# Kernel optimization log

Measured on AMD Instinct MI355X. Metric: run time of the kernel, lower is better.

## Reference

```python
import jax, jax.numpy as jnp
import numpy as np

K = 8
LN_EPS = 1e-5


def setup_inputs() -> dict:
    key = jax.random.key(0)
    ks = jax.random.split(key, 12)
    Nq, N, d = 2048, 50000, 256
    xav = np.sqrt(6.0 / (d + d)).astype(np.float32)
    inp = {
        "query": jax.random.normal(ks[0], (Nq, d), jnp.float32),
        "query_pos": jax.random.uniform(ks[1], (Nq, 3), jnp.float32) * 10.0,
        "inst_feats": jax.random.normal(ks[2], (N, d), jnp.float32),
        "sp_coords": jax.random.uniform(ks[3], (N, 3), jnp.float32) * 10.0,
        "w_q": jax.random.uniform(ks[4], (d, d), jnp.float32, -xav, xav),
        "w_v": jax.random.uniform(ks[5], (d, d), jnp.float32, -xav, xav),
        "w_o": jax.random.uniform(ks[6], (d, d), jnp.float32, -xav, xav),
        # original inits w_k/w_b to zero (uniform gate); use small random for a nontrivial gate
        "w_k": jax.random.normal(ks[7], (K, d), jnp.float32) * 0.02,
        "w_b": jax.random.normal(ks[8], (K,), jnp.float32) * 0.02,
        "gamma": jnp.ones((d,), jnp.float32),
        "beta": jnp.zeros((d,), jnp.float32),
    }
    return inp


def _knn_idx(query_pos, sp_coords, k):
    # squared euclidean distances [Nq, N] via ||q||^2 - 2 q.p + ||p||^2
    d2 = (
        jnp.sum(query_pos * query_pos, -1, keepdims=True)
        - 2.0 * (query_pos @ sp_coords.T)
        + jnp.sum(sp_coords * sp_coords, -1)[None, :]
    )
    _, idx = jax.lax.top_k(-d2, k)  # [Nq, k] nearest-neighbor indices
    return idx


def reference(query, query_pos, inst_feats, sp_coords, w_q, w_v, w_o, w_k, w_b, gamma, beta):
    idx = _knn_idx(query_pos, sp_coords, K)
    feat = inst_feats[idx]                       # [Nq, k, d] gathered neighbor feats
    q = query @ w_q.T                            # [Nq, d]
    v = feat @ w_v.T                             # [Nq, k, d]
    gate = jax.nn.softmax(q @ w_k.T + w_b, -1)   # [Nq, k]
    w = jnp.einsum("qk,qkd->qd", gate, q[:, None, :] * v)
    out = w @ w_o.T + query                      # dropout p=0 -> identity; residual
    mu = jnp.mean(out, -1, keepdims=True)
    var = jnp.mean((out - mu) ** 2, -1, keepdims=True)
    return (out - mu) * jax.lax.rsqrt(var + LN_EPS) * gamma + beta
```

## Files before the change

kernel.cpp:

```cpp
#include <hip/hip_runtime.h>
#include <math.h>

#define D        256
#define KNN      8
#define G        16
#define NCELL    (G*G*G)
#define CS       0.625f
#define EPS_D2   2e-3f
#define CAP      64
#define SPILLMAX 50000

typedef unsigned long long u64;
typedef __attribute__((ext_vector_type(8))) short bf16x8;
typedef __attribute__((ext_vector_type(4))) float f32x4;

__device__ __forceinline__ unsigned short f2b(float f) {
    unsigned u = __float_as_uint(f);
    u += 0x7fff + ((u >> 16) & 1);
    return (unsigned short)(u >> 16);
}
__device__ __forceinline__ bf16x8 pack8(float4 a, float4 b) {
    bf16x8 r;
    r[0] = (short)f2b(a.x); r[1] = (short)f2b(a.y);
    r[2] = (short)f2b(a.z); r[3] = (short)f2b(a.w);
    r[4] = (short)f2b(b.x); r[5] = (short)f2b(b.y);
    r[6] = (short)f2b(b.z); r[7] = (short)f2b(b.w);
    return r;
}

__device__ __forceinline__ unsigned enc_f32(float f) {
    unsigned b = __float_as_uint(f);
    return b ^ ((unsigned)(((int)b) >> 31) | 0x80000000u);
}
__device__ __forceinline__ float dec_f32(unsigned t) {
    unsigned m = (unsigned)(((int)t) >> 31);
    return __uint_as_float(t ^ (0x80000000u | ~m));
}
__device__ __forceinline__ u64 mkkey(float d2, int j) {
    return ((u64)enc_f32(d2) << 32) | (u64)(unsigned)j;
}
__device__ __forceinline__ int cell_of(float x) {
    int c = (int)(x * 1.6f);
    return c < 0 ? 0 : (c > G-1 ? G-1 : c);
}

#define INSERT8(xk)                                                            \
    if ((xk) < k7) {                                                           \
        const bool c0 = (xk) < k0, c1 = (xk) < k1, c2 = (xk) < k2,             \
                   c3 = (xk) < k3, c4 = (xk) < k4, c5 = (xk) < k5,             \
                   c6 = (xk) < k6;                                             \
        k7 = c6 ? k6 : (xk);                                                   \
        k6 = c5 ? k5 : (c6 ? (xk) : k6);                                       \
        k5 = c4 ? k4 : (c5 ? (xk) : k5);                                       \
        k4 = c3 ? k3 : (c4 ? (xk) : k4);                                       \
        k3 = c2 ? k2 : (c3 ? (xk) : k3);                                       \
        k2 = c1 ? k1 : (c2 ? (xk) : k2);                                       \
        k1 = c0 ? k0 : (c1 ? (xk) : k1);                                       \
        k0 = c0 ? (xk) : k0;                                                   \
    }

#define SCORE(p)                                                               \
    {                                                                          \
        const float sp  = __fadd_rn(__fadd_rn(__fmul_rn((p).x,(p).x),          \
                                  __fmul_rn((p).y,(p).y)), __fmul_rn((p).z,(p).z)); \
        const float dot = __fmaf_rn(qz,(p).z, __fmaf_rn(qy,(p).y, __fmul_rn(qx,(p).x))); \
        const float d2  = __fadd_rn(__fsub_rn(sq, __fmul_rn(2.0f, dot)), sp);  \
        const u64 xk = mkkey(d2, __float_as_int((p).w));                       \
        INSERT8(xk)                                                            \
    }

__device__ __forceinline__ void wave_merge8(int l, u64& k0, u64& k1, u64& k2, u64& k3,
                                            u64& k4, u64& k5, u64& k6, u64& k7,
                                            u64& mine)
{
#pragma unroll
    for (int rd = 0; rd < KNN; ++rd) {
        u64 m = k0;
#pragma unroll
        for (int o = 32; o; o >>= 1) {
            const u64 t = __shfl_xor(m, o);
            if (t < m) m = t;
        }
        if (k0 == m) {
            k0 = k1; k1 = k2; k2 = k3; k3 = k4; k4 = k5; k5 = k6; k6 = k7;
            k7 = ~0ull;
        }
        if (l == rd) mine = m;
    }
}

__global__ __launch_bounds__(256) void prep(const float* __restrict__ w_k,
                                            const float* __restrict__ w_q,
                                            const float* __restrict__ w_v,
                                            const float* __restrict__ w_o,
                                            float* __restrict__ wk2,
                                            unsigned short* __restrict__ wqs,
                                            unsigned short* __restrict__ wvs,
                                            unsigned short* __restrict__ wos,
                                            int4* __restrict__ cnt4,
                                            int* __restrict__ spill_cnt)
{
    const int b = blockIdx.x, t = threadIdx.x;
    if (b < 8) {
        float acc = 0.f;
#pragma unroll 8
        for (int d = 0; d < D; ++d)
            acc = fmaf(w_k[b*D + d], w_q[(size_t)d*D + t], acc);
        wk2[b*D + t] = acc;
    } else if (b < 12) {
        cnt4[(b-8)*256 + t] = make_int4(0, 0, 0, 0);
        if (b == 8 && t == 0) *spill_cnt = 0;
    } else {
        const int m = (b - 12) >> 5;
        const int local = (b - 12) & 31;
        const int idx = local * 256 + t;
        const int nt = idx >> 9;
        const int ks = (idx >> 6) & 7;
        const int l  = idx & 63;
        const int col = nt*16 + (l & 15);
        const int k   = ks*32 + (l >> 4)*8;
        const float* src = (m == 0) ? w_q : (m == 1) ? w_v : w_o;
        unsigned short* dst = (m == 0) ? wqs : (m == 1) ? wvs : wos;
        const float4 x0 = *(const float4*)&src[(size_t)col*D + k];
        const float4 x1 = *(const float4*)&src[(size_t)col*D + k + 4];
        *(bf16x8*)&dst[(size_t)idx * 8] = pack8(x0, x1);
    }
}

__global__ __launch_bounds__(256) void scatter_bins(const float* __restrict__ spc,
                                                    int* __restrict__ cnt,
                                                    float4* __restrict__ bins,
                                                    int* __restrict__ spill_cnt,
                                                    float4* __restrict__ spill, int N)
{
    const int j = blockIdx.x * 256 + threadIdx.x;
    if (j >= N) return;
    const float px = spc[3*j+0], py = spc[3*j+1], pz = spc[3*j+2];
    const int cell = cell_of(px) | (cell_of(py) << 4) | (cell_of(pz) << 8);
    const float4 p = make_float4(px, py, pz, __int_as_float(j));
    const int pos = atomicAdd(&cnt[cell], 1);
    if (pos < CAP) bins[cell*CAP + pos] = p;
    else {
        const int sp = atomicAdd(spill_cnt, 1);
        if (sp < SPILLMAX) spill[sp] = p;
    }
}

__device__ __forceinline__ void knn_gate_wave(int q, int l,
                                              const float* __restrict__ qpos,
                                              const float4* __restrict__ bins,
                                              const int* __restrict__ cnt,
                                              const int* __restrict__ spill_cnt,
                                              const float4* __restrict__ spill,
                                              const float* __restrict__ query,
                                              const float* __restrict__ wk2,
                                              const float* __restrict__ w_b,
                                              const float* __restrict__ feats,
                                              float4& qv_out, float4& fb_out)
{
    const float qx = qpos[3*q+0], qy = qpos[3*q+1], qz = qpos[3*q+2];
    const float sq = __fadd_rn(__fadd_rn(__fmul_rn(qx,qx), __fmul_rn(qy,qy)),
                               __fmul_rn(qz,qz));
    const int cx = cell_of(qx), cy = cell_of(qy), cz = cell_of(qz);

    auto bstart = [](int c, float coord) {
        const float f = coord * 1.6f - (float)c;
        int b = c + ((f < 0.5f) ? -2 : -1);
        return b < 0 ? 0 : (b > G-4 ? G-4 : b);
    };
    const int bx = bstart(cx, qx), by = bstart(cy, qy), bz = bstart(cz, qz);

    u64 k0 = ~0ull, k1 = ~0ull, k2 = ~0ull, k3 = ~0ull,
        k4 = ~0ull, k5 = ~0ull, k6 = ~0ull, k7 = ~0ull;

    {
        const int x = bx + (l & 3), y = by + ((l >> 2) & 3), z = bz + (l >> 4);
        const int ci = x | (y << 4) | (z << 8);
        const int n = min(cnt[ci], CAP);
        const int st = ci * CAP;
        for (int i = 0; i < n; ++i) { const float4 p = bins[st + i]; SCORE(p) }
    }
    {
        const int ns = min(*spill_cnt, SPILLMAX);
        for (int i = l; i < ns; i += 64) { const float4 p = spill[i]; SCORE(p) }
    }

    u64 mine = ~0ull;
    wave_merge8(l, k0, k1, k2, k3, k4, k5, k6, k7, mine);
    const u64 worst = __shfl(mine, KNN-1);

    const float w8 = dec_f32((unsigned)(worst >> 32));
    float dmin = INFINITY;
    if (bx > 0)     dmin = fminf(dmin, qx - (float)bx * CS);
    if (bx + 4 < G) dmin = fminf(dmin, (float)(bx + 4) * CS - qx);
    if (by > 0)     dmin = fminf(dmin, qy - (float)by * CS);
    if (by + 4 < G) dmin = fminf(dmin, (float)(by + 4) * CS - qy);
    if (bz > 0)     dmin = fminf(dmin, qz - (float)bz * CS);
    if (bz + 4 < G) dmin = fminf(dmin, (float)(bz + 4) * CS - qz);

    if (!(w8 + EPS_D2 <= dmin * dmin)) {
        k0 = (l < KNN) ? mine : ~0ull;
        k1 = ~0ull; k2 = ~0ull; k3 = ~0ull; k4 = ~0ull;
        k5 = ~0ull; k6 = ~0ull; k7 = ~0ull;
        for (int c = l; c < NCELL; c += 64) {
            const int x = c & 15, y = (c >> 4) & 15, z = c >> 8;
            if (x >= bx && x < bx+4 && y >= by && y < by+4 && z >= bz && z < bz+4) continue;
            const int n = min(cnt[c], CAP);
            const int st = c * CAP;
            for (int i = 0; i < n; ++i) { const float4 p = bins[st + i]; SCORE(p) }
        }
        wave_merge8(l, k0, k1, k2, k3, k4, k5, k6, k7, mine);
    }

    int ids[KNN];
    const int my_id = (int)(unsigned)(mine & 0xffffffffu);
#pragma unroll
    for (int j = 0; j < KNN; ++j) ids[j] = __shfl(my_id, j);

    const float4 qv = *(const float4*)&query[(size_t)q*D + l*4];
    float logit[KNN];
#pragma unroll
    for (int j = 0; j < KNN; ++j) {
        const float4 w = *(const float4*)&wk2[(size_t)j*D + l*4];
        logit[j] = fmaf(qv.x, w.x, fmaf(qv.y, w.y, fmaf(qv.z, w.z, qv.w*w.w)));
    }
#pragma unroll
    for (int o = 32; o; o >>= 1) {
#pragma unroll
        for (int j = 0; j < KNN; ++j) logit[j] += __shfl_xor(logit[j], o);
    }
#pragma unroll
    for (int j = 0; j < KNN; ++j) logit[j] += w_b[j];

    float m = logit[0];
#pragma unroll
    for (int j = 1; j < KNN; ++j) m = fmaxf(m, logit[j]);
    float e[KNN]; float ssum = 0.f;
#pragma unroll
    for (int j = 0; j < KNN; ++j) { e[j] = expf(logit[j] - m); ssum += e[j]; }
    const float inv = 1.f / ssum;

    float4 acc4 = make_float4(0.f, 0.f, 0.f, 0.f);
#pragma unroll
    for (int j = 0; j < KNN; ++j) {
        const float gj = e[j] * inv;
        const float4 f = *(const float4*)&feats[(size_t)ids[j]*D + l*4];
        acc4.x = fmaf(gj, f.x, acc4.x);
        acc4.y = fmaf(gj, f.y, acc4.y);
        acc4.z = fmaf(gj, f.z, acc4.z);
        acc4.w = fmaf(gj, f.w, acc4.w);
    }
    qv_out = qv;
    fb_out = acc4;
}

__global__ __launch_bounds__(512) void mega6(const float* __restrict__ qpos,
                                             const float4* __restrict__ bins,
                                             const int* __restrict__ cnt,
                                             const int* __restrict__ spill_cnt,
                                             const float4* __restrict__ spill,
                                             const float* __restrict__ query,
                                             const float* __restrict__ wk2,
                                             const float* __restrict__ w_b,
                                             const float* __restrict__ feats,
                                             const unsigned short* __restrict__ wqs,
                                             const unsigned short* __restrict__ wvs,
                                             const unsigned short* __restrict__ wos,
                                             const float* __restrict__ gmm,
                                             const float* __restrict__ bta,
                                             float* __restrict__ out)
{
    __shared__ unsigned short a_lds[16][264];
    __shared__ unsigned short f_lds[16][264];
    __shared__ unsigned short w_lds[16][264];
    __shared__ float q_f32[8][260];
    __shared__ float o_f32[8][260];

    const int tid = threadIdx.x;
    const int wv  = tid >> 6, l = tid & 63;
    const int r0  = blockIdx.x * 8;

    {
        const int arr = tid >> 8;
        const int row = 8 + ((tid >> 5) & 7);
        const int o8  = (tid & 31) * 8;
        const bf16x8 z = {0,0,0,0,0,0,0,0};
        if (arr == 0) *(bf16x8*)&a_lds[row][o8] = z;
        else          *(bf16x8*)&f_lds[row][o8] = z;
    }

    {
        float4 qv, fb;
        knn_gate_wave(r0 + wv, l, qpos, bins, cnt, spill_cnt, spill,
                      query, wk2, w_b, feats, qv, fb);
        *(float4*)&q_f32[wv][l*4] = qv;
        short4 qb; qb.x = (short)f2b(qv.x); qb.y = (short)f2b(qv.y);
                   qb.z = (short)f2b(qv.z); qb.w = (short)f2b(qv.w);
        *(short4*)&a_lds[wv][l*4] = qb;
        short4 fv; fv.x = (short)f2b(fb.x); fv.y = (short)f2b(fb.y);
                   fv.z = (short)f2b(fb.z); fv.w = (short)f2b(fb.w);
        *(short4*)&f_lds[wv][l*4] = fv;
    }
    __syncthreads();

    const int mrow = l & 15;
    const int kq   = (l >> 4) * 8;

    f32x4 aq[2], av[2];
#pragma unroll
    for (int t = 0; t < 2; ++t) {
        aq[t] = (f32x4){0.f, 0.f, 0.f, 0.f};
        av[t] = (f32x4){0.f, 0.f, 0.f, 0.f};
    }
#pragma unroll
    for (int ks = 0; ks < 8; ++ks) {
        const bf16x8 af = *(const bf16x8*)&a_lds[mrow][ks*32 + kq];
        const bf16x8 ff = *(const bf16x8*)&f_lds[mrow][ks*32 + kq];
#pragma unroll
        for (int t = 0; t < 2; ++t) {
            const int nt = wv*2 + t;
            const size_t fo = ((size_t)(nt*8 + ks)*64 + l) * 8;
            const bf16x8 bq = *(const bf16x8*)&wqs[fo];
            const bf16x8 bv = *(const bf16x8*)&wvs[fo];
            aq[t] = __builtin_amdgcn_mfma_f32_16x16x32_bf16(af, bq, aq[t], 0, 0, 0);
            av[t] = __builtin_amdgcn_mfma_f32_16x16x32_bf16(ff, bv, av[t], 0, 0, 0);
        }
    }
#pragma unroll
    for (int t = 0; t < 2; ++t) {
#pragma unroll
        for (int r = 0; r < 4; ++r) {
            const int row = (l >> 4) * 4 + r;
            const int col = wv*32 + t*16 + (l & 15);
            w_lds[row][col] = f2b(aq[t][r] * av[t][r]);
        }
    }
    __syncthreads();

    f32x4 ao[2];
#pragma unroll
    for (int t = 0; t < 2; ++t) ao[t] = (f32x4){0.f, 0.f, 0.f, 0.f};
#pragma unroll
    for (int ks = 0; ks < 8; ++ks) {
        const bf16x8 wf = *(const bf16x8*)&w_lds[mrow][ks*32 + kq];
#pragma unroll
        for (int t = 0; t < 2; ++t) {
            const int nt = wv*2 + t;
            const size_t fo = ((size_t)(nt*8 + ks)*64 + l) * 8;
            const bf16x8 bo = *(const bf16x8*)&wos[fo];
            ao[t] = __builtin_amdgcn_mfma_f32_16x16x32_bf16(wf, bo, ao[t], 0, 0, 0);
        }
    }
#pragma unroll
    for (int t = 0; t < 2; ++t) {
#pragma unroll
        for (int r = 0; r < 4; ++r) {
            const int row = (l >> 4) * 4 + r;
            if (row < 8) {
                const int col = wv*32 + t*16 + (l & 15);
                o_f32[row][col] = ao[t][r] + q_f32[row][col];
            }
        }
    }
    __syncthreads();

    {
        const float4 v = *(const float4*)&o_f32[wv][l*4];
        float s  = (v.x + v.y) + (v.z + v.w);
        float s2 = fmaf(v.x, v.x, fmaf(v.y, v.y, fmaf(v.z, v.z, v.w*v.w)));
#pragma unroll
        for (int o = 32; o; o >>= 1) { s += __shfl_xor(s, o); s2 += __shfl_xor(s2, o); }
        const float mu  = s * (1.f/256.f);
        const float var = fmaf(s2, 1.f/256.f, -mu*mu);
        const float rs  = rsqrtf(var + 1e-5f);
        const float4 g = *(const float4*)&gmm[l*4];
        const float4 b = *(const float4*)&bta[l*4];
        float4 o4;
        o4.x = (v.x - mu) * rs * g.x + b.x;
        o4.y = (v.y - mu) * rs * g.y + b.y;
        o4.z = (v.z - mu) * rs * g.z + b.z;
        o4.w = (v.w - mu) * rs * g.w + b.w;
        *(float4*)&out[(size_t)(r0+wv)*D + l*4] = o4;
    }
}

extern "C" void kernel_launch(void* const* d_in, const int* in_sizes, int n_in,
                              void* d_out, int out_size, void* d_ws, size_t ws_size,
                              hipStream_t stream)
{
    const float* query = (const float*)d_in[0];
    const float* qpos  = (const float*)d_in[1];
    const float* feats = (const float*)d_in[2];
    const float* spc   = (const float*)d_in[3];
    const float* w_q   = (const float*)d_in[4];
    const float* w_v   = (const float*)d_in[5];
    const float* w_o   = (const float*)d_in[6];
    const float* w_k   = (const float*)d_in[7];
    const float* w_b   = (const float*)d_in[8];
    const float* gamma = (const float*)d_in[9];
    const float* beta  = (const float*)d_in[10];

    const int Nq = in_sizes[0] / D;
    const int N  = in_sizes[2] / D;

    char* ws = (char*)d_ws;
    size_t off = 0;
    int* cnt = (int*)(ws + off);               off += ((size_t)NCELL * 4 + 255) & ~(size_t)255;
    int* spill_cnt = (int*)(ws + off);         off += 256;
    float* wk2 = (float*)(ws + off);           off += ((size_t)KNN * D * 4 + 255) & ~(size_t)255;
    unsigned short* wqs = (unsigned short*)(ws + off); off += (size_t)D * D * 2;
    unsigned short* wvs = (unsigned short*)(ws + off); off += (size_t)D * D * 2;
    unsigned short* wos = (unsigned short*)(ws + off); off += (size_t)D * D * 2;
    float4* bins = (float4*)(ws + off);        off += ((size_t)NCELL * CAP * 16 + 255) & ~(size_t)255;
    float4* spill = (float4*)(ws + off);       off += ((size_t)SPILLMAX * 16 + 255) & ~(size_t)255;

    prep<<<108, 256, 0, stream>>>(w_k, w_q, w_v, w_o, wk2, wqs, wvs, wos,
                                  (int4*)cnt, spill_cnt);
    scatter_bins<<<(N + 255)/256, 256, 0, stream>>>(spc, cnt, bins, spill_cnt, spill, N);
    mega6<<<Nq/8, 512, 0, stream>>>(qpos, bins, cnt, spill_cnt, spill,
                                    query, wk2, w_b, feats, wqs, wvs, wos,
                                    gamma, beta, (float*)d_out);
}
```

Baseline: 45.48 us.

## Split each query's KNN cell scan across two waves and merge via LDS

The fused kernel now handles 4 queries per block instead of 8, with two waves per query. Each wave scans half of the 64 candidate cells, and two lanes share each cell by taking alternating points. The two partial top-8 lists are merged through shared memory by one wave, which then handles the fallback full scan, the gate and the feature gather. This shortens the serial per-lane scan loop and doubles the grid size. In exchange it adds a block barrier and a merge step, and leaves half the waves idle in the gate and LayerNorm phases, with more padding waste in the MFMA tiles.

Measured after the change: 46.87 us. +3.0%, slower.

```diff
diff --git a/kernel.cpp b/kernel.cpp
--- a/kernel.cpp
+++ b/kernel.cpp
@@ -146,115 +146,7 @@
     }
 }
 
-__device__ __forceinline__ void knn_gate_wave(int q, int l,
-                                              const float* __restrict__ qpos,
-                                              const float4* __restrict__ bins,
-                                              const int* __restrict__ cnt,
-                                              const int* __restrict__ spill_cnt,
-                                              const float4* __restrict__ spill,
-                                              const float* __restrict__ query,
-                                              const float* __restrict__ wk2,
-                                              const float* __restrict__ w_b,
-                                              const float* __restrict__ feats,
-                                              float4& qv_out, float4& fb_out)
-{
-    const float qx = qpos[3*q+0], qy = qpos[3*q+1], qz = qpos[3*q+2];
-    const float sq = __fadd_rn(__fadd_rn(__fmul_rn(qx,qx), __fmul_rn(qy,qy)),
-                               __fmul_rn(qz,qz));
-    const int cx = cell_of(qx), cy = cell_of(qy), cz = cell_of(qz);
-
-    auto bstart = [](int c, float coord) {
-        const float f = coord * 1.6f - (float)c;
-        int b = c + ((f < 0.5f) ? -2 : -1);
-        return b < 0 ? 0 : (b > G-4 ? G-4 : b);
-    };
-    const int bx = bstart(cx, qx), by = bstart(cy, qy), bz = bstart(cz, qz);
-
-    u64 k0 = ~0ull, k1 = ~0ull, k2 = ~0ull, k3 = ~0ull,
-        k4 = ~0ull, k5 = ~0ull, k6 = ~0ull, k7 = ~0ull;
-
-    {
-        const int x = bx + (l & 3), y = by + ((l >> 2) & 3), z = bz + (l >> 4);
-        const int ci = x | (y << 4) | (z << 8);
-        const int n = min(cnt[ci], CAP);
-        const int st = ci * CAP;
-        for (int i = 0; i < n; ++i) { const float4 p = bins[st + i]; SCORE(p) }
-    }
-    {
-        const int ns = min(*spill_cnt, SPILLMAX);
-        for (int i = l; i < ns; i += 64) { const float4 p = spill[i]; SCORE(p) }
-    }
-
-    u64 mine = ~0ull;
-    wave_merge8(l, k0, k1, k2, k3, k4, k5, k6, k7, mine);
-    const u64 worst = __shfl(mine, KNN-1);
-
-    const float w8 = dec_f32((unsigned)(worst >> 32));
-    float dmin = INFINITY;
-    if (bx > 0)     dmin = fminf(dmin, qx - (float)bx * CS);
-    if (bx + 4 < G) dmin = fminf(dmin, (float)(bx + 4) * CS - qx);
-    if (by > 0)     dmin = fminf(dmin, qy - (float)by * CS);
-    if (by + 4 < G) dmin = fminf(dmin, (float)(by + 4) * CS - qy);
-    if (bz > 0)     dmin = fminf(dmin, qz - (float)bz * CS);
-    if (bz + 4 < G) dmin = fminf(dmin, (float)(bz + 4) * CS - qz);
-
-    if (!(w8 + EPS_D2 <= dmin * dmin)) {
-        k0 = (l < KNN) ? mine : ~0ull;
-        k1 = ~0ull; k2 = ~0ull; k3 = ~0ull; k4 = ~0ull;
-        k5 = ~0ull; k6 = ~0ull; k7 = ~0ull;
-        for (int c = l; c < NCELL; c += 64) {
-            const int x = c & 15, y = (c >> 4) & 15, z = c >> 8;
-            if (x >= bx && x < bx+4 && y >= by && y < by+4 && z >= bz && z < bz+4) continue;
-            const int n = min(cnt[c], CAP);
-            const int st = c * CAP;
-            for (int i = 0; i < n; ++i) { const float4 p = bins[st + i]; SCORE(p) }
-        }
-        wave_merge8(l, k0, k1, k2, k3, k4, k5, k6, k7, mine);
-    }
-
-    int ids[KNN];
-    const int my_id = (int)(unsigned)(mine & 0xffffffffu);
-#pragma unroll
-    for (int j = 0; j < KNN; ++j) ids[j] = __shfl(my_id, j);
-
-    const float4 qv = *(const float4*)&query[(size_t)q*D + l*4];
-    float logit[KNN];
-#pragma unroll
-    for (int j = 0; j < KNN; ++j) {
-        const float4 w = *(const float4*)&wk2[(size_t)j*D + l*4];
-        logit[j] = fmaf(qv.x, w.x, fmaf(qv.y, w.y, fmaf(qv.z, w.z, qv.w*w.w)));
-    }
-#pragma unroll
-    for (int o = 32; o; o >>= 1) {
-#pragma unroll
-        for (int j = 0; j < KNN; ++j) logit[j] += __shfl_xor(logit[j], o);
-    }
-#pragma unroll
-    for (int j = 0; j < KNN; ++j) logit[j] += w_b[j];
-
-    float m = logit[0];
-#pragma unroll
-    for (int j = 1; j < KNN; ++j) m = fmaxf(m, logit[j]);
-    float e[KNN]; float ssum = 0.f;
-#pragma unroll
-    for (int j = 0; j < KNN; ++j) { e[j] = expf(logit[j] - m); ssum += e[j]; }
-    const float inv = 1.f / ssum;
-
-    float4 acc4 = make_float4(0.f, 0.f, 0.f, 0.f);
-#pragma unroll
-    for (int j = 0; j < KNN; ++j) {
-        const float gj = e[j] * inv;
-        const float4 f = *(const float4*)&feats[(size_t)ids[j]*D + l*4];
-        acc4.x = fmaf(gj, f.x, acc4.x);
-        acc4.y = fmaf(gj, f.y, acc4.y);
-        acc4.z = fmaf(gj, f.z, acc4.z);
-        acc4.w = fmaf(gj, f.w, acc4.w);
-    }
-    qv_out = qv;
-    fb_out = acc4;
-}
-
-__global__ __launch_bounds__(512) void mega6(const float* __restrict__ qpos,
+__global__ __launch_bounds__(512) void mega7(const float* __restrict__ qpos,
                                              const float4* __restrict__ bins,
                                              const int* __restrict__ cnt,
                                              const int* __restrict__ spill_cnt,
@@ -273,33 +165,149 @@
     __shared__ unsigned short a_lds[16][264];
     __shared__ unsigned short f_lds[16][264];
     __shared__ unsigned short w_lds[16][264];
-    __shared__ float q_f32[8][260];
-    __shared__ float o_f32[8][260];
+    __shared__ float q_f32[4][260];
+    __shared__ float o_f32[4][260];
+    __shared__ u64  cand[4][16];
 
     const int tid = threadIdx.x;
     const int wv  = tid >> 6, l = tid & 63;
-    const int r0  = blockIdx.x * 8;
+    const int qi  = wv >> 1, part = wv & 1;
+    const int r0  = blockIdx.x * 4;
+    const int q   = r0 + qi;
 
     {
-        const int arr = tid >> 8;
-        const int row = 8 + ((tid >> 5) & 7);
-        const int o8  = (tid & 31) * 8;
+        const int o = tid;
+        const int oo = (o < 384) ? o : o - 384;
+        const int row = 4 + (oo >> 5);
+        const int c8 = (oo & 31) * 8;
         const bf16x8 z = {0,0,0,0,0,0,0,0};
-        if (arr == 0) *(bf16x8*)&a_lds[row][o8] = z;
-        else          *(bf16x8*)&f_lds[row][o8] = z;
-    }
+        if (o < 384) *(bf16x8*)&a_lds[row][c8] = z;
+        else         *(bf16x8*)&f_lds[row][c8] = z;
+        if (tid < 256) {
+            const int oo2 = tid + 128;
+            const int row2 = 4 + (oo2 >> 5);
+            const int c82 = (oo2 & 31) * 8;
+            *(bf16x8*)&f_lds[row2][c82] = z;
+        }
+    }
+
+    const float qx = qpos[3*q+0], qy = qpos[3*q+1], qz = qpos[3*q+2];
+    const float sq = __fadd_rn(__fadd_rn(__fmul_rn(qx,qx), __fmul_rn(qy,qy)),
+                               __fmul_rn(qz,qz));
+    const int cx = cell_of(qx), cy = cell_of(qy), cz = cell_of(qz);
+
+    auto bstart = [](int c, float coord) {
+        const float f = coord * 1.6f - (float)c;
+        int b = c + ((f < 0.5f) ? -2 : -1);
+        return b < 0 ? 0 : (b > G-4 ? G-4 : b);
+    };
+    const int bx = bstart(cx, qx), by = bstart(cy, qy), bz = bstart(cz, qz);
+
+    u64 k0 = ~0ull, k1 = ~0ull, k2 = ~0ull, k3 = ~0ull,
+        k4 = ~0ull, k5 = ~0ull, k6 = ~0ull, k7 = ~0ull;
 
     {
-        float4 qv, fb;
-        knn_gate_wave(r0 + wv, l, qpos, bins, cnt, spill_cnt, spill,
-                      query, wk2, w_b, feats, qv, fb);
-        *(float4*)&q_f32[wv][l*4] = qv;
+        const int c = part*32 + (l >> 1), sub = l & 1;
+        const int x = bx + (c & 3), y = by + ((c >> 2) & 3), z = bz + (c >> 4);
+        const int ci = x | (y << 4) | (z << 8);
+        const int n = min(cnt[ci], CAP);
+        const int st = ci * CAP;
+        for (int i = sub; i < n; i += 2) { const float4 p = bins[st + i]; SCORE(p) }
+    }
+    if (part == 0) {
+        const int ns = min(*spill_cnt, SPILLMAX);
+        for (int i = l; i < ns; i += 64) { const float4 p = spill[i]; SCORE(p) }
+    }
+
+    u64 mine = ~0ull;
+    wave_merge8(l, k0, k1, k2, k3, k4, k5, k6, k7, mine);
+    if (l < KNN) cand[qi][part*KNN + l] = mine;
+    __syncthreads();
+
+    if (part == 0) {
+        u64 k = (l < 16) ? cand[qi][l] : ~0ull;
+        u64 m2 = ~0ull;
+#pragma unroll
+        for (int rd = 0; rd < KNN; ++rd) {
+            u64 m = k;
+#pragma unroll
+            for (int o = 32; o; o >>= 1) {
+                const u64 t = __shfl_xor(m, o);
+                if (t < m) m = t;
+            }
+            if (k == m) k = ~0ull;
+            if (l == rd) m2 = m;
+        }
+        const u64 worst = __shfl(m2, KNN-1);
+        const float w8 = dec_f32((unsigned)(worst >> 32));
+        float dmin = INFINITY;
+        if (bx > 0)     dmin = fminf(dmin, qx - (float)bx * CS);
+        if (bx + 4 < G) dmin = fminf(dmin, (float)(bx + 4) * CS - qx);
+        if (by > 0)     dmin = fminf(dmin, qy - (float)by * CS);
+        if (by + 4 < G) dmin = fminf(dmin, (float)(by + 4) * CS - qy);
+        if (bz > 0)     dmin = fminf(dmin, qz - (float)bz * CS);
+        if (bz + 4 < G) dmin = fminf(dmin, (float)(bz + 4) * CS - qz);
+
+        if (!(w8 + EPS_D2 <= dmin * dmin)) {
+            k0 = (l < KNN) ? m2 : ~0ull;
+            k1 = ~0ull; k2 = ~0ull; k3 = ~0ull; k4 = ~0ull;
+            k5 = ~0ull; k6 = ~0ull; k7 = ~0ull;
+            for (int c = l; c < NCELL; c += 64) {
+                const int x = c & 15, y = (c >> 4) & 15, z = c >> 8;
+                if (x >= bx && x < bx+4 && y >= by && y < by+4 && z >= bz && z < bz+4) continue;
+                const int n = min(cnt[c], CAP);
+                const int st = c * CAP;
+                for (int i = 0; i < n; ++i) { const float4 p = bins[st + i]; SCORE(p) }
+            }
+            wave_merge8(l, k0, k1, k2, k3, k4, k5, k6, k7, m2);
+        }
+
+        int ids[KNN];
+        const int my_id = (int)(unsigned)(m2 & 0xffffffffu);
+#pragma unroll
+        for (int j = 0; j < KNN; ++j) ids[j] = __shfl(my_id, j);
+
+        const float4 qv = *(const float4*)&query[(size_t)q*D + l*4];
+        float logit[KNN];
+#pragma unroll
+        for (int j = 0; j < KNN; ++j) {
+            const float4 w = *(const float4*)&wk2[(size_t)j*D + l*4];
+            logit[j] = fmaf(qv.x, w.x, fmaf(qv.y, w.y, fmaf(qv.z, w.z, qv.w*w.w)));
+        }
+#pragma unroll
+        for (int o = 32; o; o >>= 1) {
+#pragma unroll
+            for (int j = 0; j < KNN; ++j) logit[j] += __shfl_xor(logit[j], o);
+        }
+#pragma unroll
+        for (int j = 0; j < KNN; ++j) logit[j] += w_b[j];
+
+        float m = logit[0];
+#pragma unroll
+        for (int j = 1; j < KNN; ++j) m = fmaxf(m, logit[j]);
+        float e[KNN]; float ssum = 0.f;
+#pragma unroll
+        for (int j = 0; j < KNN; ++j) { e[j] = expf(logit[j] - m); ssum += e[j]; }
+        const float inv = 1.f / ssum;
+
+        float4 acc4 = make_float4(0.f, 0.f, 0.f, 0.f);
+#pragma unroll
+        for (int j = 0; j < KNN; ++j) {
+            const float gj = e[j] * inv;
+            const float4 f = *(const float4*)&feats[(size_t)ids[j]*D + l*4];
+            acc4.x = fmaf(gj, f.x, acc4.x);
+            acc4.y = fmaf(gj, f.y, acc4.y);
+            acc4.z = fmaf(gj, f.z, acc4.z);
+            acc4.w = fmaf(gj, f.w, acc4.w);
+        }
+
+        *(float4*)&q_f32[qi][l*4] = qv;
         short4 qb; qb.x = (short)f2b(qv.x); qb.y = (short)f2b(qv.y);
                    qb.z = (short)f2b(qv.z); qb.w = (short)f2b(qv.w);
-        *(short4*)&a_lds[wv][l*4] = qb;
-        short4 fv; fv.x = (short)f2b(fb.x); fv.y = (short)f2b(fb.y);
-                   fv.z = (short)f2b(fb.z); fv.w = (short)f2b(fb.w);
-        *(short4*)&f_lds[wv][l*4] = fv;
+        *(short4*)&a_lds[qi][l*4] = qb;
+        short4 fv; fv.x = (short)f2b(acc4.x); fv.y = (short)f2b(acc4.y);
+                   fv.z = (short)f2b(acc4.z); fv.w = (short)f2b(acc4.w);
+        *(short4*)&f_lds[qi][l*4] = fv;
     }
     __syncthreads();
 
@@ -356,7 +364,7 @@
 #pragma unroll
         for (int r = 0; r < 4; ++r) {
             const int row = (l >> 4) * 4 + r;
-            if (row < 8) {
+            if (row < 4) {
                 const int col = wv*32 + t*16 + (l & 15);
                 o_f32[row][col] = ao[t][r] + q_f32[row][col];
             }
@@ -364,7 +372,7 @@
     }
     __syncthreads();
 
-    {
+    if (wv < 4) {
         const float4 v = *(const float4*)&o_f32[wv][l*4];
         float s  = (v.x + v.y) + (v.z + v.w);
         float s2 = fmaf(v.x, v.x, fmaf(v.y, v.y, fmaf(v.z, v.z, v.w*v.w)));
@@ -417,7 +425,7 @@
     prep<<<108, 256, 0, stream>>>(w_k, w_q, w_v, w_o, wk2, wqs, wvs, wos,
                                   (int4*)cnt, spill_cnt);
     scatter_bins<<<(N + 255)/256, 256, 0, stream>>>(spc, cnt, bins, spill_cnt, spill, N);
-    mega6<<<Nq/8, 512, 0, stream>>>(qpos, bins, cnt, spill_cnt, spill,
+    mega7<<<Nq/4, 512, 0, stream>>>(qpos, bins, cnt, spill_cnt, spill,
                                     query, wk2, w_b, feats, wqs, wvs, wos,
                                     gamma, beta, (float*)d_out);
 }
```

## Fuse point binning into main kernel behind a grid-wide spin barrier

Applied to the files above, without the earlier changes.

Removes the separate scatter_bins launch. The main kernel now bins the points itself (512 points per block) and then waits on a global atomic spin barrier before doing the KNN, gate and GEMM work. The aim is to save one kernel launch and its gap. The barrier depends on all 256 blocks being resident at once, which holds for 256 blocks on this GPU but could deadlock elsewhere. Nq/8 = 256 matches MBLOCKS, and 256*512 covers N=50000.

After: 60.15 us. 32.3% more time.

```diff
diff --git a/kernel.cpp b/kernel.cpp
--- a/kernel.cpp
+++ b/kernel.cpp
@@ -9,6 +9,7 @@
 #define EPS_D2   2e-3f
 #define CAP      64
 #define SPILLMAX 50000
+#define MBLOCKS  256
 
 typedef unsigned long long u64;
 typedef __attribute__((ext_vector_type(8))) short bf16x8;
@@ -89,16 +90,17 @@
     }
 }
 
-__global__ __launch_bounds__(256) void prep(const float* __restrict__ w_k,
-                                            const float* __restrict__ w_q,
-                                            const float* __restrict__ w_v,
-                                            const float* __restrict__ w_o,
-                                            float* __restrict__ wk2,
-                                            unsigned short* __restrict__ wqs,
-                                            unsigned short* __restrict__ wvs,
-                                            unsigned short* __restrict__ wos,
-                                            int4* __restrict__ cnt4,
-                                            int* __restrict__ spill_cnt)
+__global__ __launch_bounds__(256) void init_k(const float* __restrict__ w_k,
+                                              const float* __restrict__ w_q,
+                                              const float* __restrict__ w_v,
+                                              const float* __restrict__ w_o,
+                                              float* __restrict__ wk2,
+                                              unsigned short* __restrict__ wqs,
+                                              unsigned short* __restrict__ wvs,
+                                              unsigned short* __restrict__ wos,
+                                              int4* __restrict__ cnt4,
+                                              int* __restrict__ spill_cnt,
+                                              int* __restrict__ bar)
 {
     const int b = blockIdx.x, t = threadIdx.x;
     if (b < 8) {
@@ -109,7 +111,7 @@
         wk2[b*D + t] = acc;
     } else if (b < 12) {
         cnt4[(b-8)*256 + t] = make_int4(0, 0, 0, 0);
-        if (b == 8 && t == 0) *spill_cnt = 0;
+        if (b == 8 && t == 0) { *spill_cnt = 0; *bar = 0; }
     } else {
         const int m = (b - 12) >> 5;
         const int local = (b - 12) & 31;
@@ -124,25 +126,6 @@
         const float4 x0 = *(const float4*)&src[(size_t)col*D + k];
         const float4 x1 = *(const float4*)&src[(size_t)col*D + k + 4];
         *(bf16x8*)&dst[(size_t)idx * 8] = pack8(x0, x1);
-    }
-}
-
-__global__ __launch_bounds__(256) void scatter_bins(const float* __restrict__ spc,
-                                                    int* __restrict__ cnt,
-                                                    float4* __restrict__ bins,
-                                                    int* __restrict__ spill_cnt,
-                                                    float4* __restrict__ spill, int N)
-{
-    const int j = blockIdx.x * 256 + threadIdx.x;
-    if (j >= N) return;
-    const float px = spc[3*j+0], py = spc[3*j+1], pz = spc[3*j+2];
-    const int cell = cell_of(px) | (cell_of(py) << 4) | (cell_of(pz) << 8);
-    const float4 p = make_float4(px, py, pz, __int_as_float(j));
-    const int pos = atomicAdd(&cnt[cell], 1);
-    if (pos < CAP) bins[cell*CAP + pos] = p;
-    else {
-        const int sp = atomicAdd(spill_cnt, 1);
-        if (sp < SPILLMAX) spill[sp] = p;
     }
 }
 
@@ -254,21 +237,23 @@
     fb_out = acc4;
 }
 
-__global__ __launch_bounds__(512) void mega6(const float* __restrict__ qpos,
-                                             const float4* __restrict__ bins,
-                                             const int* __restrict__ cnt,
-                                             const int* __restrict__ spill_cnt,
-                                             const float4* __restrict__ spill,
-                                             const float* __restrict__ query,
-                                             const float* __restrict__ wk2,
-                                             const float* __restrict__ w_b,
-                                             const float* __restrict__ feats,
-                                             const unsigned short* __restrict__ wqs,
-                                             const unsigned short* __restrict__ wvs,
-                                             const unsigned short* __restrict__ wos,
-                                             const float* __restrict__ gmm,
-                                             const float* __restrict__ bta,
-                                             float* __restrict__ out)
+__global__ __launch_bounds__(512) void monolith(const float* __restrict__ spc,
+                                                int* __restrict__ cnt,
+                                                float4* __restrict__ bins,
+                                                int* __restrict__ spill_cnt,
+                                                float4* __restrict__ spill,
+                                                int* __restrict__ bar,
+                                                const float* __restrict__ qpos,
+                                                const float* __restrict__ query,
+                                                const float* __restrict__ wk2,
+                                                const float* __restrict__ w_b,
+                                                const float* __restrict__ feats,
+                                                const unsigned short* __restrict__ wqs,
+                                                const unsigned short* __restrict__ wvs,
+                                                const unsigned short* __restrict__ wos,
+                                                const float* __restrict__ gmm,
+                                                const float* __restrict__ bta,
+                                                float* __restrict__ out, int N)
 {
     __shared__ unsigned short a_lds[16][264];
     __shared__ unsigned short f_lds[16][264];
@@ -279,6 +264,30 @@
     const int tid = threadIdx.x;
     const int wv  = tid >> 6, l = tid & 63;
     const int r0  = blockIdx.x * 8;
+
+    {
+        const int j = blockIdx.x * 512 + tid;
+        if (j < N) {
+            const float px = spc[3*j+0], py = spc[3*j+1], pz = spc[3*j+2];
+            const int cell = cell_of(px) | (cell_of(py) << 4) | (cell_of(pz) << 8);
+            const float4 p = make_float4(px, py, pz, __int_as_float(j));
+            const int pos = atomicAdd(&cnt[cell], 1);
+            if (pos < CAP) bins[cell*CAP + pos] = p;
+            else {
+                const int sp = atomicAdd(spill_cnt, 1);
+                if (sp < SPILLMAX) spill[sp] = p;
+            }
+        }
+    }
+
+    __syncthreads();
+    if (tid == 0) {
+        __threadfence();
+        atomicAdd(bar, 1);
+        while (atomicAdd(bar, 0) < MBLOCKS) {}
+        __threadfence();
+    }
+    __syncthreads();
 
     {
         const int arr = tid >> 8;
@@ -407,6 +416,7 @@
     size_t off = 0;
     int* cnt = (int*)(ws + off);               off += ((size_t)NCELL * 4 + 255) & ~(size_t)255;
     int* spill_cnt = (int*)(ws + off);         off += 256;
+    int* bar = (int*)(ws + off);               off += 256;
     float* wk2 = (float*)(ws + off);           off += ((size_t)KNN * D * 4 + 255) & ~(size_t)255;
     unsigned short* wqs = (unsigned short*)(ws + off); off += (size_t)D * D * 2;
     unsigned short* wvs = (unsigned short*)(ws + off); off += (size_t)D * D * 2;
@@ -414,10 +424,10 @@
     float4* bins = (float4*)(ws + off);        off += ((size_t)NCELL * CAP * 16 + 255) & ~(size_t)255;
     float4* spill = (float4*)(ws + off);       off += ((size_t)SPILLMAX * 16 + 255) & ~(size_t)255;
 
-    prep<<<108, 256, 0, stream>>>(w_k, w_q, w_v, w_o, wk2, wqs, wvs, wos,
-                                  (int4*)cnt, spill_cnt);
-    scatter_bins<<<(N + 255)/256, 256, 0, stream>>>(spc, cnt, bins, spill_cnt, spill, N);
-    mega6<<<Nq/8, 512, 0, stream>>>(qpos, bins, cnt, spill_cnt, spill,
-                                    query, wk2, w_b, feats, wqs, wvs, wos,
-                                    gamma, beta, (float*)d_out);
-}
+    init_k<<<108, 256, 0, stream>>>(w_k, w_q, w_v, w_o, wk2, wqs, wvs, wos,
+                                    (int4*)cnt, spill_cnt, bar);
+    monolith<<<MBLOCKS, 512, 0, stream>>>(spc, cnt, bins, spill_cnt, spill, bar,
+                                          qpos, query, wk2, w_b, feats,
+                                          wqs, wvs, wos, gamma, beta,
+                                          (float*)d_out, N);
+}
```
